# Kernel tuning notes

Hardware: AMD Instinct MI355X
Metric: run time of the kernel (lower is better)

## Reference

```python
import jax, jax.numpy as jnp
import numpy as np

B, T, N, M, D = 4, 64, 16, 8, 512

def setup_inputs() -> dict:
    key = jax.random.key(0)
    ks = jax.random.split(key, 7)
    s = 1.0 / np.sqrt(D)
    return {
        "x": jax.random.normal(ks[0], (B, T, N, M, D), dtype=jnp.float32),
        "Wq": jax.random.normal(ks[1], (D, D), dtype=jnp.float32) * s,
        "bq": jax.random.normal(ks[2], (D,), dtype=jnp.float32) * s,
        "Wk": jax.random.normal(ks[3], (D, D), dtype=jnp.float32) * s,
        "bk": jax.random.normal(ks[4], (D,), dtype=jnp.float32) * s,
        "Wv": jax.random.normal(ks[5], (D, D), dtype=jnp.float32) * s,
        "bv": jax.random.normal(ks[6], (D,), dtype=jnp.float32) * s,
    }

def reference(x, Wq, bq, Wk, bk, Wv, bv):
    # Linear projections (torch Linear: y = x @ W^T + b)
    Q = jnp.einsum('btnmd,ed->btnme', x, Wq) + bq
    K = jnp.einsum('btnmd,ed->btnme', x, Wk) + bk
    V = jnp.einsum('btnmd,ed->btnme', x, Wv) + bv
    scale = 1.0 / jnp.sqrt(jnp.asarray(Q.shape[-1], Q.dtype))
    # contract over batch b AND feature d -> shared attention over modality axis m
    attn_score = jnp.einsum('btnmd,btnkd->tnmk', Q, K) * scale  # [t,n,m,m]
    attn_weight = jax.nn.softmax(attn_score, axis=-1)
    return jnp.einsum('tnmk,btnkd->btnmd', attn_weight, V)
```

## Files before the change

kernel.cpp:

```cpp
#include <hip/hip_runtime.h>

#define Bb 4
#define Tt 64
#define Nn 16
#define Mm 8
#define Dd 512
#define RR 32
#define QSTR 536
#define VOFF 270336

typedef __attribute__((ext_vector_type(8))) short bf16x8;
typedef __attribute__((ext_vector_type(16))) float f32x16;

__device__ __forceinline__ unsigned short f2bf(float f) {
    union { float f; unsigned int u; } v; v.f = f;
    unsigned int r = (v.u + 0x7fffu + ((v.u >> 16) & 1u)) >> 16;
    return (unsigned short)r;
}
__device__ __forceinline__ float bf2f(unsigned short h) {
    union { unsigned int u; float f; } v; v.u = ((unsigned int)h) << 16;
    return v.f;
}

__global__ __launch_bounds__(256) void pack_kernel(
    const float* __restrict__ Wq, const float* __restrict__ Wk,
    const float* __restrict__ Wv, const float* __restrict__ bq,
    unsigned short* __restrict__ Wb)
{
    const int tid = threadIdx.x;
    if (blockIdx.x >= 256) {
        int idx = (blockIdx.x - 256) * 256 + tid;
        int o = idx << 2;
        int j  = o & 7;
        int n  = (o >> 3) & 31;
        int hi = (o >> 8) & 1;
        int ekk = o >> 9;
        int kk = ekk & 31;
        int e  = ekk >> 5;
        int row = e * 32 + n;
        int d = kk * 16 + hi * 8 + j;
        float4 v = *(const float4*)(Wv + row * Dd + d);
        ushort4 o4;
        o4.x = f2bf(v.x); o4.y = f2bf(v.y); o4.z = f2bf(v.z); o4.w = f2bf(v.w);
        *(ushort4*)(Wb + VOFF + o) = o4;
        return;
    }

    const int eT = blockIdx.x & 15;
    const int dT = blockIdx.x >> 4;
    const int wave = tid >> 6, lane = tid & 63;
    const int arow = lane & 31, h = lane >> 5;

    f32x16 acc;
    #pragma unroll
    for (int r = 0; r < 16; ++r) acc[r] = 0.f;

    #pragma unroll
    for (int s = 0; s < 8; ++s) {
        int n0 = (wave * 8 + s) * 16;
        bf16x8 af, bfr;
        #pragma unroll
        for (int j = 0; j < 8; ++j) {
            int n = n0 + h * 8 + j;
            af[j]  = (short)f2bf(Wq[n * Dd + dT * 32 + arow]);
            bfr[j] = (short)f2bf(Wk[n * Dd + eT * 32 + arow]);
        }
        acc = __builtin_amdgcn_mfma_f32_32x32x16_bf16(af, bfr, acc, 0, 0, 0);
    }

    __shared__ float red[4][1024];
    #pragma unroll
    for (int r = 0; r < 16; ++r) {
        int row = (r & 3) + 8 * (r >> 2) + 4 * h;
        red[wave][row * 32 + arow] = acc[r];
    }
    __syncthreads();

    #pragma unroll
    for (int i = 0; i < 4; ++i) {
        int el = i * 256 + tid;
        int dp = el >> 5, ep = el & 31;
        float v = red[0][el] + red[1][el] + red[2][el] + red[3][el];
        int d = dT * 32 + dp;
        int kkg = d >> 4, hh = (d >> 3) & 1, jj = d & 7;
        Wb[(long)(eT * 33 + kkg) * 512 + ((hh * 32 + ep) << 3) + jj] = f2bf(v);
    }

    if (dT == 0) {
        int ep = tid & 31, strip = tid >> 5;
        float c = 0.f;
        #pragma unroll 8
        for (int n = strip * 64; n < strip * 64 + 64; ++n)
            c += bf2f(f2bf(Wk[n * Dd + eT * 32 + ep])) * bq[n];
        __syncthreads();
        red[0][tid] = c;
        long b32 = (long)(eT * 33 + 32) << 9;
        Wb[b32 + tid] = 0; Wb[b32 + 256 + tid] = 0;
        __syncthreads();
        if (tid < 32) {
            float s = 0.f;
            #pragma unroll
            for (int k = 0; k < 8; ++k) s += red[0][k * 32 + tid];
            Wb[b32 + (tid << 3)] = f2bf(s);
        }
    }
}

__global__ __launch_bounds__(1024, 4) void fused_attn_kernel(
    const float* __restrict__ x, const unsigned short* __restrict__ Wb,
    const float* __restrict__ bv, float* __restrict__ out)
{
    __shared__ unsigned short lds_x[2][RR * QSTR];
    __shared__ float lds_s[2][64];

    const int tid = threadIdx.x;
    const int lane = tid & 63;
    const int wave = tid >> 6;
    const int arow = lane & 31;
    const int ahalf = lane >> 5;
    const int l5 = lane & 31;

    const int gi0 = blockIdx.x << 1;
    const int t = gi0 >> 4;
    const int n0 = gi0 & 15;
    const int rot = (blockIdx.x * 7) & 31;

    const unsigned short* wb = Wb + (long)wave * (33 * 512) + (lane << 3);
    #define KOF(s) ((s) + rot >= 32 ? (s) + rot - 32 : (s) + rot)

    bf16x8 pf[4];
    #pragma unroll
    for (int i = 0; i < 4; ++i)
        pf[i] = *(const bf16x8*)(wb + KOF(i) * 512);

    if (tid < 128) lds_s[tid >> 6][tid & 63] = 0.f;

    #pragma unroll
    for (int i = 0; i < 8; ++i) {
        int fi = i * 1024 + tid;
        int g = fi >> 12;
        int rem = fi & 4095;
        int row = rem >> 7;
        int d = (rem & 127) << 2;
        int b = row >> 3, m = row & 7;
        float4 v = *(const float4*)(x + ((((long)(b * Tt + t)) * Nn + (n0 + g)) * Mm + m) * Dd + d);
        ushort4 o;
        o.x = f2bf(v.x); o.y = f2bf(v.y); o.z = f2bf(v.z); o.w = f2bf(v.w);
        *(ushort4*)(&lds_x[g][row * QSTR + d]) = o;
    }
    if (tid < 64) {
        int g = tid >> 5, row = tid & 31;
        unsigned short* p = &lds_x[g][row * QSTR + 512];
        ushort4 one = {0x3F80, 0, 0, 0}, zz = {0, 0, 0, 0};
        *(ushort4*)(p) = one; *(ushort4*)(p + 4) = zz;
        *(ushort4*)(p + 8) = zz; *(ushort4*)(p + 12) = zz;
    }
    __syncthreads();

    const unsigned short* abase0 = &lds_x[0][arow * QSTR + (ahalf << 3)];
    const unsigned short* abase1 = &lds_x[1][arow * QSTR + (ahalf << 3)];

    f32x16 aY0, aY1;
    #pragma unroll
    for (int r = 0; r < 16; ++r) { aY0[r] = 0.f; aY1[r] = 0.f; }

    #pragma unroll
    for (int s = 0; s < 33; ++s) {
        int kk = (s < 32) ? KOF(s) : 32;
        bf16x8 bf = pf[s & 3];
        if (s + 4 <= 32) {
            int kn = (s + 4 < 32) ? KOF(s + 4) : 32;
            pf[s & 3] = *(const bf16x8*)(wb + kn * 512);
        }
        bf16x8 a0 = *(const bf16x8*)(abase0 + kk * 16);
        bf16x8 a1 = *(const bf16x8*)(abase1 + kk * 16);
        aY0 = __builtin_amdgcn_mfma_f32_32x32x16_bf16(a0, bf, aY0, 0, 0, 0);
        aY1 = __builtin_amdgcn_mfma_f32_32x32x16_bf16(a1, bf, aY1, 0, 0, 0);
    }

    const unsigned short* vb = Wb + VOFF + ((long)wave << 14) + (lane << 3);
    bf16x8 pv[4];
    pv[0] = *(const bf16x8*)(vb + ((0 + rot) & 31) * 512);
    pv[1] = *(const bf16x8*)(vb + ((1 + rot) & 31) * 512);
    pv[2] = *(const bf16x8*)(vb + ((2 + rot) & 31) * 512);
    pv[3] = *(const bf16x8*)(vb + ((3 + rot) & 31) * 512);

    const int ecol = (wave << 5) + l5;
    #pragma unroll
    for (int g = 0; g < 2; ++g) {
        const f32x16& aY = g ? aY1 : aY0;
        float p[32];
        #pragma unroll
        for (int i = 0; i < 32; ++i) p[i] = 0.f;
        #pragma unroll
        for (int b = 0; b < 4; ++b) {
            float xc[8];
            #pragma unroll
            for (int k = 0; k < 8; ++k)
                xc[k] = bf2f(lds_x[g][(b * 8 + k) * QSTR + ecol]);
            #pragma unroll
            for (int mm = 0; mm < 4; ++mm) {
                float yv = aY[b * 4 + mm];
                #pragma unroll
                for (int k = 0; k < 8; ++k) p[mm * 8 + k] += yv * xc[k];
            }
        }
        const bool b0 = (lane & 1) != 0;
        const bool b1 = (lane & 2) != 0;
        const bool b2 = (lane & 4) != 0;
        const bool b3 = (lane & 8) != 0;
        const bool b4 = (lane & 16) != 0;
        float q16[16];
        #pragma unroll
        for (int i = 0; i < 16; ++i) {
            float keep = b0 ? p[2 * i + 1] : p[2 * i];
            float send = b0 ? p[2 * i] : p[2 * i + 1];
            q16[i] = keep + __shfl_xor(send, 1);
        }
        float q8[8];
        #pragma unroll
        for (int i = 0; i < 8; ++i) {
            float keep = b1 ? q16[2 * i + 1] : q16[2 * i];
            float send = b1 ? q16[2 * i] : q16[2 * i + 1];
            q8[i] = keep + __shfl_xor(send, 2);
        }
        float q4[4];
        #pragma unroll
        for (int i = 0; i < 4; ++i) {
            float keep = b2 ? q8[2 * i + 1] : q8[2 * i];
            float send = b2 ? q8[2 * i] : q8[2 * i + 1];
            q4[i] = keep + __shfl_xor(send, 4);
        }
        float q2[2];
        #pragma unroll
        for (int i = 0; i < 2; ++i) {
            float keep = b3 ? q4[2 * i + 1] : q4[2 * i];
            float send = b3 ? q4[2 * i] : q4[2 * i + 1];
            q2[i] = keep + __shfl_xor(send, 8);
        }
        float sval = (b4 ? q2[1] : q2[0]) + __shfl_xor(b4 ? q2[0] : q2[1], 16);
        int k = l5 & 7, mm = l5 >> 3;
        int m = mm + 4 * ahalf;
        atomicAdd(&lds_s[g][m * 8 + k], sval);
    }

    f32x16 aZ0, aZ1;
    #pragma unroll
    for (int r = 0; r < 16; ++r) { aZ0[r] = 0.f; aZ1[r] = 0.f; }
    #pragma unroll
    for (int s = 0; s < 32; ++s) {
        int kk = (s + rot) & 31;
        bf16x8 wvf = pv[s & 3];
        if (s + 4 < 32) pv[s & 3] = *(const bf16x8*)(vb + (((s + 4 + rot) & 31)) * 512);
        bf16x8 a0 = *(const bf16x8*)(abase0 + kk * 16);
        bf16x8 a1 = *(const bf16x8*)(abase1 + kk * 16);
        aZ0 = __builtin_amdgcn_mfma_f32_32x32x16_bf16(a0, wvf, aZ0, 0, 0, 0);
        aZ1 = __builtin_amdgcn_mfma_f32_32x32x16_bf16(a1, wvf, aZ1, 0, 0, 0);
    }
    __syncthreads();

    if (tid < 128) {
        int g = tid >> 6;
        int p = tid & 63;
        float s = lds_s[g][p] * 0.04419417382415922f;
        float mx = s;
        mx = fmaxf(mx, __shfl_xor(mx, 1));
        mx = fmaxf(mx, __shfl_xor(mx, 2));
        mx = fmaxf(mx, __shfl_xor(mx, 4));
        float e = __expf(s - mx);
        float sum = e;
        sum += __shfl_xor(sum, 1);
        sum += __shfl_xor(sum, 2);
        sum += __shfl_xor(sum, 4);
        lds_s[g][p] = e / sum;
    }
    __syncthreads();

    {
        int f = (wave << 5) + arow;
        float bvv = bv[f];
        float* o0 = out + f;
        #pragma unroll
        for (int g = 0; g < 2; ++g) {
            const f32x16& z = g ? aZ1 : aZ0;
            float zs[16];
            #pragma unroll
            for (int r = 0; r < 16; ++r) zs[r] = __shfl_xor(z[r], 32);
            #pragma unroll
            for (int j = 0; j < 4; ++j) {
                int m = j + 4 * ahalf;
                float4 pA = *(const float4*)&lds_s[g][m * 8 + 4 * ahalf];
                float4 pB = *(const float4*)&lds_s[g][m * 8 + 4 * (1 - ahalf)];
                #pragma unroll
                for (int b = 0; b < 4; ++b) {
                    int r0 = 4 * b;
                    float o = pA.x * z[r0]  + pA.y * z[r0 + 1]
                            + pA.z * z[r0 + 2] + pA.w * z[r0 + 3]
                            + pB.x * zs[r0] + pB.y * zs[r0 + 1]
                            + pB.z * zs[r0 + 2] + pB.w * zs[r0 + 3];
                    long base = ((((long)(b * Tt + t)) * Nn + (n0 + g)) * Mm + m) * Dd;
                    o0[base] = o + bvv;
                }
            }
        }
    }
    #undef KOF
}

extern "C" void kernel_launch(void* const* d_in, const int* in_sizes, int n_in,
                              void* d_out, int out_size, void* d_ws, size_t ws_size,
                              hipStream_t stream) {
    const float* x  = (const float*)d_in[0];
    const float* Wq = (const float*)d_in[1];
    const float* bq = (const float*)d_in[2];
    const float* Wk = (const float*)d_in[3];
    const float* Wv = (const float*)d_in[5];
    const float* bv = (const float*)d_in[6];
    float* out = (float*)d_out;
    unsigned short* Wb = (unsigned short*)d_ws;

    pack_kernel<<<512, 256, 0, stream>>>(Wq, Wk, Wv, bq, Wb);
    fused_attn_kernel<<<Tt * Nn / 2, 1024, 0, stream>>>(x, Wb, bv, out);
}
```

Before: 171.8 us.

## Process two group pairs per block with prefetch of next x tile into LDS

Each block now handles four (t,n) groups in two iterations instead of two, halving the grid to 256 blocks. While the first pair is computed, the x data for the second pair is loaded from global memory into registers and converted into a second LDS buffer, so the load latency overlaps MFMA work. The cost is doubled LDS use (about 137KB), which limits occupancy to one block per CU, plus fewer blocks than CUs and higher register pressure from the held prefetch values.

Result: no change. 173.0 us (+0.7%).

```diff
diff --git a/kernel.cpp b/kernel.cpp
--- a/kernel.cpp
+++ b/kernel.cpp
@@ -110,8 +110,8 @@
     const float* __restrict__ x, const unsigned short* __restrict__ Wb,
     const float* __restrict__ bv, float* __restrict__ out)
 {
-    __shared__ unsigned short lds_x[2][RR * QSTR];
-    __shared__ float lds_s[2][64];
+    __shared__ unsigned short lds_x[2][2][RR * QSTR];
+    __shared__ float lds_s[2][2][64];
 
     const int tid = threadIdx.x;
     const int lane = tid & 63;
@@ -120,12 +120,12 @@
     const int ahalf = lane >> 5;
     const int l5 = lane & 31;
 
-    const int gi0 = blockIdx.x << 1;
-    const int t = gi0 >> 4;
-    const int n0 = gi0 & 15;
+    const int t = blockIdx.x >> 2;
+    const int nb = (blockIdx.x & 3) << 2;
     const int rot = (blockIdx.x * 7) & 31;
 
     const unsigned short* wb = Wb + (long)wave * (33 * 512) + (lane << 3);
+    const unsigned short* vb = Wb + VOFF + ((long)wave << 14) + (lane << 3);
     #define KOF(s) ((s) + rot >= 32 ? (s) + rot - 32 : (s) + rot)
 
     bf16x8 pf[4];
@@ -133,7 +133,7 @@
     for (int i = 0; i < 4; ++i)
         pf[i] = *(const bf16x8*)(wb + KOF(i) * 512);
 
-    if (tid < 128) lds_s[tid >> 6][tid & 63] = 0.f;
+    if (tid < 256) ((float*)lds_s)[tid] = 0.f;
 
     #pragma unroll
     for (int i = 0; i < 8; ++i) {
@@ -143,163 +143,226 @@
         int row = rem >> 7;
         int d = (rem & 127) << 2;
         int b = row >> 3, m = row & 7;
-        float4 v = *(const float4*)(x + ((((long)(b * Tt + t)) * Nn + (n0 + g)) * Mm + m) * Dd + d);
+        float4 v = *(const float4*)(x + ((((long)(b * Tt + t)) * Nn + (nb + g)) * Mm + m) * Dd + d);
         ushort4 o;
         o.x = f2bf(v.x); o.y = f2bf(v.y); o.z = f2bf(v.z); o.w = f2bf(v.w);
-        *(ushort4*)(&lds_x[g][row * QSTR + d]) = o;
+        *(ushort4*)(&lds_x[0][g][row * QSTR + d]) = o;
     }
     if (tid < 64) {
         int g = tid >> 5, row = tid & 31;
-        unsigned short* p = &lds_x[g][row * QSTR + 512];
+        unsigned short* p = &lds_x[0][g][row * QSTR + 512];
         ushort4 one = {0x3F80, 0, 0, 0}, zz = {0, 0, 0, 0};
         *(ushort4*)(p) = one; *(ushort4*)(p + 4) = zz;
         *(ushort4*)(p + 8) = zz; *(ushort4*)(p + 12) = zz;
     }
     __syncthreads();
 
-    const unsigned short* abase0 = &lds_x[0][arow * QSTR + (ahalf << 3)];
-    const unsigned short* abase1 = &lds_x[1][arow * QSTR + (ahalf << 3)];
-
-    f32x16 aY0, aY1;
-    #pragma unroll
-    for (int r = 0; r < 16; ++r) { aY0[r] = 0.f; aY1[r] = 0.f; }
-
-    #pragma unroll
-    for (int s = 0; s < 33; ++s) {
-        int kk = (s < 32) ? KOF(s) : 32;
-        bf16x8 bf = pf[s & 3];
-        if (s + 4 <= 32) {
-            int kn = (s + 4 < 32) ? KOF(s + 4) : 32;
-            pf[s & 3] = *(const bf16x8*)(wb + kn * 512);
-        }
-        bf16x8 a0 = *(const bf16x8*)(abase0 + kk * 16);
-        bf16x8 a1 = *(const bf16x8*)(abase1 + kk * 16);
-        aY0 = __builtin_amdgcn_mfma_f32_32x32x16_bf16(a0, bf, aY0, 0, 0, 0);
-        aY1 = __builtin_amdgcn_mfma_f32_32x32x16_bf16(a1, bf, aY1, 0, 0, 0);
-    }
-
-    const unsigned short* vb = Wb + VOFF + ((long)wave << 14) + (lane << 3);
-    bf16x8 pv[4];
-    pv[0] = *(const bf16x8*)(vb + ((0 + rot) & 31) * 512);
-    pv[1] = *(const bf16x8*)(vb + ((1 + rot) & 31) * 512);
-    pv[2] = *(const bf16x8*)(vb + ((2 + rot) & 31) * 512);
-    pv[3] = *(const bf16x8*)(vb + ((3 + rot) & 31) * 512);
-
-    const int ecol = (wave << 5) + l5;
-    #pragma unroll
-    for (int g = 0; g < 2; ++g) {
-        const f32x16& aY = g ? aY1 : aY0;
-        float p[32];
-        #pragma unroll
-        for (int i = 0; i < 32; ++i) p[i] = 0.f;
-        #pragma unroll
-        for (int b = 0; b < 4; ++b) {
-            float xc[8];
-            #pragma unroll
-            for (int k = 0; k < 8; ++k)
-                xc[k] = bf2f(lds_x[g][(b * 8 + k) * QSTR + ecol]);
-            #pragma unroll
-            for (int mm = 0; mm < 4; ++mm) {
-                float yv = aY[b * 4 + mm];
+    #pragma unroll
+    for (int it = 0; it < 2; ++it) {
+        const int n0 = nb + it * 2;
+        float4 sxA[4], sxB[4];
+
+        const unsigned short* abase0 = &lds_x[it][0][arow * QSTR + (ahalf << 3)];
+        const unsigned short* abase1 = &lds_x[it][1][arow * QSTR + (ahalf << 3)];
+
+        f32x16 aY0, aY1;
+        #pragma unroll
+        for (int r = 0; r < 16; ++r) { aY0[r] = 0.f; aY1[r] = 0.f; }
+
+        #pragma unroll
+        for (int s = 0; s < 33; ++s) {
+            int kk = (s < 32) ? KOF(s) : 32;
+            bf16x8 bf = pf[s & 3];
+            if (s + 4 <= 32) {
+                int kn = (s + 4 < 32) ? KOF(s + 4) : 32;
+                pf[s & 3] = *(const bf16x8*)(wb + kn * 512);
+            }
+            bf16x8 a0 = *(const bf16x8*)(abase0 + kk * 16);
+            bf16x8 a1 = *(const bf16x8*)(abase1 + kk * 16);
+            aY0 = __builtin_amdgcn_mfma_f32_32x32x16_bf16(a0, bf, aY0, 0, 0, 0);
+            aY1 = __builtin_amdgcn_mfma_f32_32x32x16_bf16(a1, bf, aY1, 0, 0, 0);
+        }
+
+        bf16x8 pv[4];
+        pv[0] = *(const bf16x8*)(vb + ((0 + rot) & 31) * 512);
+        pv[1] = *(const bf16x8*)(vb + ((1 + rot) & 31) * 512);
+        pv[2] = *(const bf16x8*)(vb + ((2 + rot) & 31) * 512);
+        pv[3] = *(const bf16x8*)(vb + ((3 + rot) & 31) * 512);
+
+        if (it == 0) {
+            #pragma unroll
+            for (int i = 0; i < 4; ++i) {
+                int fi = i * 1024 + tid;
+                int row = (fi & 4095) >> 7;
+                int d = (fi & 127) << 2;
+                int b = row >> 3, m = row & 7;
+                sxA[i] = *(const float4*)(x + ((((long)(b * Tt + t)) * Nn + (nb + 2)) * Mm + m) * Dd + d);
+            }
+        }
+
+        const int ecol = (wave << 5) + l5;
+        #pragma unroll
+        for (int g = 0; g < 2; ++g) {
+            const f32x16& aY = g ? aY1 : aY0;
+            float p[32];
+            #pragma unroll
+            for (int i = 0; i < 32; ++i) p[i] = 0.f;
+            #pragma unroll
+            for (int b = 0; b < 4; ++b) {
+                float xc[8];
                 #pragma unroll
-                for (int k = 0; k < 8; ++k) p[mm * 8 + k] += yv * xc[k];
-            }
-        }
-        const bool b0 = (lane & 1) != 0;
-        const bool b1 = (lane & 2) != 0;
-        const bool b2 = (lane & 4) != 0;
-        const bool b3 = (lane & 8) != 0;
-        const bool b4 = (lane & 16) != 0;
-        float q16[16];
-        #pragma unroll
-        for (int i = 0; i < 16; ++i) {
-            float keep = b0 ? p[2 * i + 1] : p[2 * i];
-            float send = b0 ? p[2 * i] : p[2 * i + 1];
-            q16[i] = keep + __shfl_xor(send, 1);
-        }
-        float q8[8];
-        #pragma unroll
-        for (int i = 0; i < 8; ++i) {
-            float keep = b1 ? q16[2 * i + 1] : q16[2 * i];
-            float send = b1 ? q16[2 * i] : q16[2 * i + 1];
-            q8[i] = keep + __shfl_xor(send, 2);
-        }
-        float q4[4];
-        #pragma unroll
-        for (int i = 0; i < 4; ++i) {
-            float keep = b2 ? q8[2 * i + 1] : q8[2 * i];
-            float send = b2 ? q8[2 * i] : q8[2 * i + 1];
-            q4[i] = keep + __shfl_xor(send, 4);
-        }
-        float q2[2];
-        #pragma unroll
-        for (int i = 0; i < 2; ++i) {
-            float keep = b3 ? q4[2 * i + 1] : q4[2 * i];
-            float send = b3 ? q4[2 * i] : q4[2 * i + 1];
-            q2[i] = keep + __shfl_xor(send, 8);
-        }
-        float sval = (b4 ? q2[1] : q2[0]) + __shfl_xor(b4 ? q2[0] : q2[1], 16);
-        int k = l5 & 7, mm = l5 >> 3;
-        int m = mm + 4 * ahalf;
-        atomicAdd(&lds_s[g][m * 8 + k], sval);
-    }
-
-    f32x16 aZ0, aZ1;
-    #pragma unroll
-    for (int r = 0; r < 16; ++r) { aZ0[r] = 0.f; aZ1[r] = 0.f; }
-    #pragma unroll
-    for (int s = 0; s < 32; ++s) {
-        int kk = (s + rot) & 31;
-        bf16x8 wvf = pv[s & 3];
-        if (s + 4 < 32) pv[s & 3] = *(const bf16x8*)(vb + (((s + 4 + rot) & 31)) * 512);
-        bf16x8 a0 = *(const bf16x8*)(abase0 + kk * 16);
-        bf16x8 a1 = *(const bf16x8*)(abase1 + kk * 16);
-        aZ0 = __builtin_amdgcn_mfma_f32_32x32x16_bf16(a0, wvf, aZ0, 0, 0, 0);
-        aZ1 = __builtin_amdgcn_mfma_f32_32x32x16_bf16(a1, wvf, aZ1, 0, 0, 0);
-    }
-    __syncthreads();
-
-    if (tid < 128) {
-        int g = tid >> 6;
-        int p = tid & 63;
-        float s = lds_s[g][p] * 0.04419417382415922f;
-        float mx = s;
-        mx = fmaxf(mx, __shfl_xor(mx, 1));
-        mx = fmaxf(mx, __shfl_xor(mx, 2));
-        mx = fmaxf(mx, __shfl_xor(mx, 4));
-        float e = __expf(s - mx);
-        float sum = e;
-        sum += __shfl_xor(sum, 1);
-        sum += __shfl_xor(sum, 2);
-        sum += __shfl_xor(sum, 4);
-        lds_s[g][p] = e / sum;
-    }
-    __syncthreads();
-
-    {
-        int f = (wave << 5) + arow;
-        float bvv = bv[f];
-        float* o0 = out + f;
-        #pragma unroll
-        for (int g = 0; g < 2; ++g) {
-            const f32x16& z = g ? aZ1 : aZ0;
-            float zs[16];
-            #pragma unroll
-            for (int r = 0; r < 16; ++r) zs[r] = __shfl_xor(z[r], 32);
-            #pragma unroll
-            for (int j = 0; j < 4; ++j) {
-                int m = j + 4 * ahalf;
-                float4 pA = *(const float4*)&lds_s[g][m * 8 + 4 * ahalf];
-                float4 pB = *(const float4*)&lds_s[g][m * 8 + 4 * (1 - ahalf)];
+                for (int k = 0; k < 8; ++k)
+                    xc[k] = bf2f(lds_x[it][g][(b * 8 + k) * QSTR + ecol]);
                 #pragma unroll
-                for (int b = 0; b < 4; ++b) {
-                    int r0 = 4 * b;
-                    float o = pA.x * z[r0]  + pA.y * z[r0 + 1]
-                            + pA.z * z[r0 + 2] + pA.w * z[r0 + 3]
-                            + pB.x * zs[r0] + pB.y * zs[r0 + 1]
-                            + pB.z * zs[r0 + 2] + pB.w * zs[r0 + 3];
-                    long base = ((((long)(b * Tt + t)) * Nn + (n0 + g)) * Mm + m) * Dd;
-                    o0[base] = o + bvv;
+                for (int mm = 0; mm < 4; ++mm) {
+                    float yv = aY[b * 4 + mm];
+                    #pragma unroll
+                    for (int k = 0; k < 8; ++k) p[mm * 8 + k] += yv * xc[k];
+                }
+            }
+            const bool b0 = (lane & 1) != 0;
+            const bool b1 = (lane & 2) != 0;
+            const bool b2 = (lane & 4) != 0;
+            const bool b3 = (lane & 8) != 0;
+            const bool b4 = (lane & 16) != 0;
+            float q16[16];
+            #pragma unroll
+            for (int i = 0; i < 16; ++i) {
+                float keep = b0 ? p[2 * i + 1] : p[2 * i];
+                float send = b0 ? p[2 * i] : p[2 * i + 1];
+                q16[i] = keep + __shfl_xor(send, 1);
+            }
+            float q8[8];
+            #pragma unroll
+            for (int i = 0; i < 8; ++i) {
+                float keep = b1 ? q16[2 * i + 1] : q16[2 * i];
+                float send = b1 ? q16[2 * i] : q16[2 * i + 1];
+                q8[i] = keep + __shfl_xor(send, 2);
+            }
+            float q4[4];
+            #pragma unroll
+            for (int i = 0; i < 4; ++i) {
+                float keep = b2 ? q8[2 * i + 1] : q8[2 * i];
+                float send = b2 ? q8[2 * i] : q8[2 * i + 1];
+                q4[i] = keep + __shfl_xor(send, 4);
+            }
+            float q2[2];
+            #pragma unroll
+            for (int i = 0; i < 2; ++i) {
+                float keep = b3 ? q4[2 * i + 1] : q4[2 * i];
+                float send = b3 ? q4[2 * i] : q4[2 * i + 1];
+                q2[i] = keep + __shfl_xor(send, 8);
+            }
+            float sval = (b4 ? q2[1] : q2[0]) + __shfl_xor(b4 ? q2[0] : q2[1], 16);
+            int k = l5 & 7, mm = l5 >> 3;
+            int m = mm + 4 * ahalf;
+            atomicAdd(&lds_s[it][g][m * 8 + k], sval);
+        }
+
+        if (it == 0) {
+            #pragma unroll
+            for (int i = 0; i < 4; ++i) {
+                int fi = i * 1024 + tid;
+                int row = (fi & 4095) >> 7;
+                int d = (fi & 127) << 2;
+                ushort4 o;
+                o.x = f2bf(sxA[i].x); o.y = f2bf(sxA[i].y);
+                o.z = f2bf(sxA[i].z); o.w = f2bf(sxA[i].w);
+                *(ushort4*)(&lds_x[1][0][row * QSTR + d]) = o;
+            }
+            #pragma unroll
+            for (int i = 0; i < 4; ++i) {
+                int fi = i * 1024 + tid;
+                int row = (fi & 4095) >> 7;
+                int d = (fi & 127) << 2;
+                int b = row >> 3, m = row & 7;
+                sxB[i] = *(const float4*)(x + ((((long)(b * Tt + t)) * Nn + (nb + 3)) * Mm + m) * Dd + d);
+            }
+        }
+
+        f32x16 aZ0, aZ1;
+        #pragma unroll
+        for (int r = 0; r < 16; ++r) { aZ0[r] = 0.f; aZ1[r] = 0.f; }
+        #pragma unroll
+        for (int s = 0; s < 32; ++s) {
+            int kk = (s + rot) & 31;
+            bf16x8 wvf = pv[s & 3];
+            if (s + 4 < 32) pv[s & 3] = *(const bf16x8*)(vb + (((s + 4 + rot) & 31)) * 512);
+            bf16x8 a0 = *(const bf16x8*)(abase0 + kk * 16);
+            bf16x8 a1 = *(const bf16x8*)(abase1 + kk * 16);
+            aZ0 = __builtin_amdgcn_mfma_f32_32x32x16_bf16(a0, wvf, aZ0, 0, 0, 0);
+            aZ1 = __builtin_amdgcn_mfma_f32_32x32x16_bf16(a1, wvf, aZ1, 0, 0, 0);
+        }
+
+        if (it == 0) {
+            #pragma unroll
+            for (int i = 0; i < 4; ++i) {
+                int fi = i * 1024 + tid;
+                int row = (fi & 4095) >> 7;
+                int d = (fi & 127) << 2;
+                ushort4 o;
+                o.x = f2bf(sxB[i].x); o.y = f2bf(sxB[i].y);
+                o.z = f2bf(sxB[i].z); o.w = f2bf(sxB[i].w);
+                *(ushort4*)(&lds_x[1][1][row * QSTR + d]) = o;
+            }
+            if (tid < 64) {
+                int g = tid >> 5, row = tid & 31;
+                unsigned short* p = &lds_x[1][g][row * QSTR + 512];
+                ushort4 one = {0x3F80, 0, 0, 0}, zz = {0, 0, 0, 0};
+                *(ushort4*)(p) = one; *(ushort4*)(p + 4) = zz;
+                *(ushort4*)(p + 8) = zz; *(ushort4*)(p + 12) = zz;
+            }
+        }
+        __syncthreads();
+
+        if (tid < 128) {
+            int g = tid >> 6;
+            int p = tid & 63;
+            float s = lds_s[it][g][p] * 0.04419417382415922f;
+            float mx = s;
+            mx = fmaxf(mx, __shfl_xor(mx, 1));
+            mx = fmaxf(mx, __shfl_xor(mx, 2));
+            mx = fmaxf(mx, __shfl_xor(mx, 4));
+            float e = __expf(s - mx);
+            float sum = e;
+            sum += __shfl_xor(sum, 1);
+            sum += __shfl_xor(sum, 2);
+            sum += __shfl_xor(sum, 4);
+            lds_s[it][g][p] = e / sum;
+        }
+        __syncthreads();
+
+        if (it == 0) {
+            #pragma unroll
+            for (int i = 0; i < 4; ++i)
+                pf[i] = *(const bf16x8*)(wb + KOF(i) * 512);
+        }
+
+        {
+            int f = (wave << 5) + arow;
+            float bvv = bv[f];
+            float* o0 = out + f;
+            #pragma unroll
+            for (int g = 0; g < 2; ++g) {
+                const f32x16& z = g ? aZ1 : aZ0;
+                float zs[16];
+                #pragma unroll
+                for (int r = 0; r < 16; ++r) zs[r] = __shfl_xor(z[r], 32);
+                #pragma unroll
+                for (int j = 0; j < 4; ++j) {
+                    int m = j + 4 * ahalf;
+                    float4 pA = *(const float4*)&lds_s[it][g][m * 8 + 4 * ahalf];
+                    float4 pB = *(const float4*)&lds_s[it][g][m * 8 + 4 * (1 - ahalf)];
+                    #pragma unroll
+                    for (int b = 0; b < 4; ++b) {
+                        int r0 = 4 * b;
+                        float o = pA.x * z[r0]  + pA.y * z[r0 + 1]
+                                + pA.z * z[r0 + 2] + pA.w * z[r0 + 3]
+                                + pB.x * zs[r0] + pB.y * zs[r0 + 1]
+                                + pB.z * zs[r0 + 2] + pB.w * zs[r0 + 3];
+                        long base = ((((long)(b * Tt + t)) * Nn + (n0 + g)) * Mm + m) * Dd;
+                        o0[base] = o + bvv;
+                    }
                 }
             }
         }
@@ -320,5 +383,5 @@
     unsigned short* Wb = (unsigned short*)d_ws;
 
     pack_kernel<<<512, 256, 0, stream>>>(Wq, Wk, Wv, bq, Wb);
-    fused_attn_kernel<<<Tt * Nn / 2, 1024, 0, stream>>>(x, Wb, bv, out);
-}
+    fused_attn_kernel<<<Tt * Nn / 4, 1024, 0, stream>>>(x, Wb, bv, out);
+}
```
